# Kernel optimization log

Measured on AMD Instinct MI355X. Metric: run time of the kernel, lower is better.

## Reference

```python
import jax, jax.numpy as jnp
import numpy as np


def setup_inputs() -> dict:
    key = jax.random.key(0)
    k0, k1, k2, k3 = jax.random.split(key, 4)
    B, N, C = 4, 1024, 64
    x = jax.random.normal(k0, (B, N, C), dtype=jnp.float32)
    # torch nn.Linear weights are [out, in]; all projections are bias-free
    W1 = jax.random.normal(k1, (C, C), dtype=jnp.float32) * (1.0 / np.sqrt(C))
    W2 = jax.random.normal(k2, (C, C), dtype=jnp.float32) * (1.0 / np.sqrt(C))
    w3 = jax.random.normal(k3, (C,), dtype=jnp.float32) * (1.0 / np.sqrt(C))
    return {"x": x, "W1": W1, "W2": W2, "w3": w3}


def reference(x, W1, W2, w3):
    # x: [B, N, C]; torch Linear: y = x @ W.T
    x1 = jnp.einsum("bnc,dc->bnd", x, W1)  # [B, N, C]
    x2 = jnp.einsum("bnc,dc->bnd", x, W2)  # [B, N, C]
    # broadcast-add over node pairs, tanh, project C -> 1: [B, N, N]
    combined = jnp.tanh(x1[:, :, None, :] + x2[:, None, :, :])  # [B, N, N, C]
    att = jnp.einsum("bijc,c->bij", combined, w3)
    return jax.nn.softmax(att, axis=-1)
```

## Files before the change

kernel.cpp:

```cpp
#include <hip/hip_runtime.h>
#include <hip/hip_bf16.h>


#define BATCH 4
#define NN    1024
#define CC    64
#define TI    4
#define BLK   512
#define NCH   (NN / BLK)
#define PP    65
#define PROWS 16

__device__ __forceinline__ float fast_exp2(float x) {
#if __has_builtin(__builtin_amdgcn_exp2f)
    return __builtin_amdgcn_exp2f(x);
#else
    return exp2f(x);
#endif
}
__device__ __forceinline__ float fast_rcp(float x) {
#if __has_builtin(__builtin_amdgcn_rcpf)
    return __builtin_amdgcn_rcpf(x);
#else
    return 1.0f / x;
#endif
}

__global__ __launch_bounds__(256) void proj_kernel(
    const float* __restrict__ x, const float* __restrict__ W1,
    const float* __restrict__ W2, float* __restrict__ e1p,
    float* __restrict__ e2p) {
    __shared__ float w1t[CC * PP];
    __shared__ float w2t[CC * PP];
    __shared__ float xs[PROWS * CC];

    const int tid = threadIdx.x;
    const int r0  = blockIdx.x * PROWS;
    {
        const float4* __restrict__ W1v = (const float4*)W1;
        const float4* __restrict__ W2v = (const float4*)W2;
#pragma unroll
        for (int k = 0; k < 4; ++k) {
            const int fi = k * 256 + tid;
            const int r  = fi >> 4;
            const int c4 = (fi & 15) * 4;
            float4 a = W1v[fi], b = W2v[fi];
            w1t[(c4 + 0) * PP + r] = a.x; w1t[(c4 + 1) * PP + r] = a.y;
            w1t[(c4 + 2) * PP + r] = a.z; w1t[(c4 + 3) * PP + r] = a.w;
            w2t[(c4 + 0) * PP + r] = b.x; w2t[(c4 + 1) * PP + r] = b.y;
            w2t[(c4 + 2) * PP + r] = b.z; w2t[(c4 + 3) * PP + r] = b.w;
        }
        const int rr = tid >> 6, c = tid & 63;
#pragma unroll
        for (int k = 0; k < 4; ++k) {
            const int r = k * 4 + rr;
            xs[r * CC + c] = x[(size_t)(r0 + r) * CC + c];
        }
    }
    __syncthreads();

    const int w    = tid >> 6;
    const int lane = tid & 63;
    const int rb   = w * 4;

    float a1[4] = {0.f, 0.f, 0.f, 0.f};
    float a2[4] = {0.f, 0.f, 0.f, 0.f};
#pragma unroll
    for (int c = 0; c < CC; ++c) {
        const float w1v = w1t[c * PP + lane];
        const float w2v = w2t[c * PP + lane];
        const float x0 = xs[(rb + 0) * CC + c];
        const float x1 = xs[(rb + 1) * CC + c];
        const float x2v = xs[(rb + 2) * CC + c];
        const float x3 = xs[(rb + 3) * CC + c];
        a1[0] = fmaf(x0, w1v, a1[0]);  a2[0] = fmaf(x0, w2v, a2[0]);
        a1[1] = fmaf(x1, w1v, a1[1]);  a2[1] = fmaf(x1, w2v, a2[1]);
        a1[2] = fmaf(x2v, w1v, a1[2]); a2[2] = fmaf(x2v, w2v, a2[2]);
        a1[3] = fmaf(x3, w1v, a1[3]);  a2[3] = fmaf(x3, w2v, a2[3]);
    }
    const float K2 = 2.8853900817779268f;
#pragma unroll
    for (int rr = 0; rr < 4; ++rr) {
        const size_t r = (size_t)(r0 + rb + rr);
        e1p[r * CC + lane] = fast_exp2(fminf(a1[rr] * K2, 15.f));
        e2p[r * CC + lane] = fast_exp2(fminf(a2[rr] * K2, 15.f));
    }
}

__device__ __forceinline__ void step2(float e1a, float e1b, float e2,
                                      float wc, float2& acc) {
    float da = fmaf(e1a, e2, 1.f);
    float db = fmaf(e1b, e2, 1.f);
    float r  = fast_rcp(da * db);
    float t  = wc * r;
    acc.x = fmaf(db, t, acc.x);
    acc.y = fmaf(da, t, acc.y);
}

__global__ __launch_bounds__(BLK) void attn_kernel(
    const float* __restrict__ e1p, const float* __restrict__ e2p,
    const float* __restrict__ w3, float* __restrict__ out) {
    __shared__ float e1t[CC * TI];
    __shared__ float att_lds[TI * NN];

    const int tid = threadIdx.x;
    const int bi  = blockIdx.x;
    const int b   = bi >> 8;
    const int i0  = (bi & 255) * TI;

    if (tid < CC * TI) {
        const int ii = tid >> 6, c = tid & 63;
        e1t[c * TI + ii] = e1p[(size_t)((b << 10) + i0 + ii) * CC + c];
    }
    __syncthreads();

    const float4* __restrict__ w3q = (const float4*)w3;
    float sumw3 = 0.f;
#pragma unroll
    for (int q = 0; q < 16; ++q) {
        float4 t = w3q[q];
        sumw3 += (t.x + t.y) + (t.z + t.w);
    }

    const float* __restrict__ e2b = e2p + ((size_t)b << 10) * CC;
    const float4* e1t4 = (const float4*)e1t;

#pragma unroll 1
    for (int ch = 0; ch < NCH; ++ch) {
        const int j = ch * BLK + tid;
        const float4* __restrict__ row = (const float4*)(e2b + (size_t)j * CC);

        float2 accA = {0.f, 0.f};
        float2 accB = {0.f, 0.f};

#pragma unroll 1
        for (int ct = 0; ct < 4; ++ct) {
#pragma unroll
            for (int q = 0; q < 4; ++q) {
                const float4 ev2 = row[ct * 4 + q];
                const float4 wv  = w3q[ct * 4 + q];
                const float ea[4] = {ev2.x, ev2.y, ev2.z, ev2.w};
                const float wa[4] = {wv.x, wv.y, wv.z, wv.w};
#pragma unroll
                for (int m = 0; m < 4; ++m) {
                    const int c = ct * 16 + q * 4 + m;
                    const float4 ev = e1t4[c];
                    step2(ev.x, ev.y, ea[m], wa[m], accA);
                    step2(ev.z, ev.w, ea[m], wa[m], accB);
                }
            }
        }
        att_lds[0 * NN + j] = fmaf(-2.f, accA.x, sumw3);
        att_lds[1 * NN + j] = fmaf(-2.f, accA.y, sumw3);
        att_lds[2 * NN + j] = fmaf(-2.f, accB.x, sumw3);
        att_lds[3 * NN + j] = fmaf(-2.f, accB.y, sumw3);
    }
    __syncthreads();

    {
        const int w    = tid >> 6;
        const int lane = tid & 63;
        if (w < TI) {
            float v[16];
            float m = -3.4e38f;
#pragma unroll
            for (int k = 0; k < 16; ++k) {
                v[k] = att_lds[w * NN + k * 64 + lane];
                m = fmaxf(m, v[k]);
            }
#pragma unroll
            for (int off = 32; off >= 1; off >>= 1)
                m = fmaxf(m, __shfl_xor(m, off));
            const float L2E = 1.4426950408889634f;
            float s = 0.f;
#pragma unroll
            for (int k = 0; k < 16; ++k) {
                v[k] = fast_exp2((v[k] - m) * L2E);
                s += v[k];
            }
#pragma unroll
            for (int off = 32; off >= 1; off >>= 1)
                s += __shfl_xor(s, off);
            const float rs = fast_rcp(s);
            float* __restrict__ orow = out + (((size_t)(b << 10) + (i0 + w)) << 10);
#pragma unroll
            for (int k = 0; k < 16; ++k) orow[k * 64 + lane] = v[k] * rs;
        }
    }
}

extern "C" void kernel_launch(void* const* d_in, const int* in_sizes, int n_in,
                              void* d_out, int out_size, void* d_ws, size_t ws_size,
                              hipStream_t stream) {
    const float* x  = (const float*)d_in[0];
    const float* W1 = (const float*)d_in[1];
    const float* W2 = (const float*)d_in[2];
    const float* w3 = (const float*)d_in[3];
    float* outp = (float*)d_out;

    float* e1p = (float*)d_ws;
    float* e2p = e1p + (size_t)BATCH * NN * CC;

    proj_kernel<<<dim3(BATCH * NN / PROWS), dim3(256), 0, stream>>>(x, W1, W2, e1p, e2p);
    attn_kernel<<<dim3(BATCH * NN / TI), dim3(BLK), 0, stream>>>(e1p, e2p, w3, outp);
}
```

Baseline: 102.7 us.

## Process two j rows per thread and read e1 rows directly via uniform loads

The attention kernel now handles both 512-wide j chunks in a single pass, so each thread accumulates two j rows at once and reuses the loaded e1 and w3 values across them. The shared-memory staging of the four e1 rows and its barrier are dropped. Those rows are read straight from global memory with wave-uniform addresses, which the compiler can turn into scalar loads. This cuts LDS traffic and loop overhead and exposes more independent work per thread, at the cost of more live registers.

```diff
diff --git a/kernel.cpp b/kernel.cpp
--- a/kernel.cpp
+++ b/kernel.cpp
@@ -7,7 +7,6 @@
 #define CC    64
 #define TI    4
 #define BLK   512
-#define NCH   (NN / BLK)
 #define PP    65
 #define PROWS 16
 
@@ -100,7 +99,6 @@
 __global__ __launch_bounds__(BLK) void attn_kernel(
     const float* __restrict__ e1p, const float* __restrict__ e2p,
     const float* __restrict__ w3, float* __restrict__ out) {
-    __shared__ float e1t[CC * TI];
     __shared__ float att_lds[TI * NN];
 
     const int tid = threadIdx.x;
@@ -108,13 +106,16 @@
     const int b   = bi >> 8;
     const int i0  = (bi & 255) * TI;
 
-    if (tid < CC * TI) {
-        const int ii = tid >> 6, c = tid & 63;
-        e1t[c * TI + ii] = e1p[(size_t)((b << 10) + i0 + ii) * CC + c];
-    }
-    __syncthreads();
-
+    const float4* __restrict__ e1r0 =
+        (const float4*)(e1p + ((size_t)(b << 10) + i0 + 0) * CC);
+    const float4* __restrict__ e1r1 =
+        (const float4*)(e1p + ((size_t)(b << 10) + i0 + 1) * CC);
+    const float4* __restrict__ e1r2 =
+        (const float4*)(e1p + ((size_t)(b << 10) + i0 + 2) * CC);
+    const float4* __restrict__ e1r3 =
+        (const float4*)(e1p + ((size_t)(b << 10) + i0 + 3) * CC);
     const float4* __restrict__ w3q = (const float4*)w3;
+
     float sumw3 = 0.f;
 #pragma unroll
     for (int q = 0; q < 16; ++q) {
@@ -123,38 +124,40 @@
     }
 
     const float* __restrict__ e2b = e2p + ((size_t)b << 10) * CC;
-    const float4* e1t4 = (const float4*)e1t;
+    const int j0 = tid, j1 = tid + BLK;
+    const float4* __restrict__ rowA = (const float4*)(e2b + (size_t)j0 * CC);
+    const float4* __restrict__ rowB = (const float4*)(e2b + (size_t)j1 * CC);
+
+    float2 aA = {0.f, 0.f}, bA = {0.f, 0.f};
+    float2 aB = {0.f, 0.f}, bB = {0.f, 0.f};
 
 #pragma unroll 1
-    for (int ch = 0; ch < NCH; ++ch) {
-        const int j = ch * BLK + tid;
-        const float4* __restrict__ row = (const float4*)(e2b + (size_t)j * CC);
-
-        float2 accA = {0.f, 0.f};
-        float2 accB = {0.f, 0.f};
-
-#pragma unroll 1
-        for (int ct = 0; ct < 4; ++ct) {
-#pragma unroll
-            for (int q = 0; q < 4; ++q) {
-                const float4 ev2 = row[ct * 4 + q];
-                const float4 wv  = w3q[ct * 4 + q];
-                const float ea[4] = {ev2.x, ev2.y, ev2.z, ev2.w};
-                const float wa[4] = {wv.x, wv.y, wv.z, wv.w};
-#pragma unroll
-                for (int m = 0; m < 4; ++m) {
-                    const int c = ct * 16 + q * 4 + m;
-                    const float4 ev = e1t4[c];
-                    step2(ev.x, ev.y, ea[m], wa[m], accA);
-                    step2(ev.z, ev.w, ea[m], wa[m], accB);
-                }
-            }
-        }
-        att_lds[0 * NN + j] = fmaf(-2.f, accA.x, sumw3);
-        att_lds[1 * NN + j] = fmaf(-2.f, accA.y, sumw3);
-        att_lds[2 * NN + j] = fmaf(-2.f, accB.x, sumw3);
-        att_lds[3 * NN + j] = fmaf(-2.f, accB.y, sumw3);
-    }
+    for (int ct = 0; ct < 16; ++ct) {
+        const float4 eA = rowA[ct];
+        const float4 eB = rowB[ct];
+        const float4 p0 = e1r0[ct];
+        const float4 p1 = e1r1[ct];
+        const float4 p2 = e1r2[ct];
+        const float4 p3 = e1r3[ct];
+        const float4 wv = w3q[ct];
+        step2(p0.x, p1.x, eA.x, wv.x, aA);  step2(p2.x, p3.x, eA.x, wv.x, bA);
+        step2(p0.x, p1.x, eB.x, wv.x, aB);  step2(p2.x, p3.x, eB.x, wv.x, bB);
+        step2(p0.y, p1.y, eA.y, wv.y, aA);  step2(p2.y, p3.y, eA.y, wv.y, bA);
+        step2(p0.y, p1.y, eB.y, wv.y, aB);  step2(p2.y, p3.y, eB.y, wv.y, bB);
+        step2(p0.z, p1.z, eA.z, wv.z, aA);  step2(p2.z, p3.z, eA.z, wv.z, bA);
+        step2(p0.z, p1.z, eB.z, wv.z, aB);  step2(p2.z, p3.z, eB.z, wv.z, bB);
+        step2(p0.w, p1.w, eA.w, wv.w, aA);  step2(p2.w, p3.w, eA.w, wv.w, bA);
+        step2(p0.w, p1.w, eB.w, wv.w, aB);  step2(p2.w, p3.w, eB.w, wv.w, bB);
+    }
+
+    att_lds[0 * NN + j0] = fmaf(-2.f, aA.x, sumw3);
+    att_lds[1 * NN + j0] = fmaf(-2.f, aA.y, sumw3);
+    att_lds[2 * NN + j0] = fmaf(-2.f, bA.x, sumw3);
+    att_lds[3 * NN + j0] = fmaf(-2.f, bA.y, sumw3);
+    att_lds[0 * NN + j1] = fmaf(-2.f, aB.x, sumw3);
+    att_lds[1 * NN + j1] = fmaf(-2.f, aB.y, sumw3);
+    att_lds[2 * NN + j1] = fmaf(-2.f, bB.x, sumw3);
+    att_lds[3 * NN + j1] = fmaf(-2.f, bB.y, sumw3);
     __syncthreads();
 
     {
```

After: 132.2 us. +28.7%, slower.

## Register-block four j rows per thread with prefetch and 256-thread blocks

Applied to the files above, without the earlier changes.

Shrinks the attention block to 256 threads, each computing four j columns at once, so every LDS read of e1 and w3 is reused across four e2 rows. The loads for the next channel group are issued one iteration ahead as a software prefetch. w3 is now staged in LDS and all four wavefronts take part in the softmax. The aim is fewer LDS reads per unit of math and better latency hiding, at the cost of many more live registers, which may lower occupancy.

```diff
diff --git a/kernel.cpp b/kernel.cpp
--- a/kernel.cpp
+++ b/kernel.cpp
@@ -6,8 +6,8 @@
 #define NN    1024
 #define CC    64
 #define TI    4
-#define BLK   512
-#define NCH   (NN / BLK)
+#define BLK   256
+#define J4    4
 #define PP    65
 #define PROWS 16
 
@@ -97,10 +97,11 @@
     acc.y = fmaf(da, t, acc.y);
 }
 
-__global__ __launch_bounds__(BLK) void attn_kernel(
+__global__ __launch_bounds__(BLK, 4) void attn_kernel(
     const float* __restrict__ e1p, const float* __restrict__ e2p,
     const float* __restrict__ w3, float* __restrict__ out) {
     __shared__ float e1t[CC * TI];
+    __shared__ float w3s[CC];
     __shared__ float att_lds[TI * NN];
 
     const int tid = threadIdx.x;
@@ -108,9 +109,10 @@
     const int b   = bi >> 8;
     const int i0  = (bi & 255) * TI;
 
-    if (tid < CC * TI) {
+    {
         const int ii = tid >> 6, c = tid & 63;
         e1t[c * TI + ii] = e1p[(size_t)((b << 10) + i0 + ii) * CC + c];
+        if (tid < CC) w3s[tid] = w3[tid];
     }
     __syncthreads();
 
@@ -123,69 +125,94 @@
     }
 
     const float* __restrict__ e2b = e2p + ((size_t)b << 10) * CC;
+    const float4* __restrict__ row0 = (const float4*)(e2b + (size_t)(tid          ) * CC);
+    const float4* __restrict__ row1 = (const float4*)(e2b + (size_t)(tid + 1 * BLK) * CC);
+    const float4* __restrict__ row2 = (const float4*)(e2b + (size_t)(tid + 2 * BLK) * CC);
+    const float4* __restrict__ row3 = (const float4*)(e2b + (size_t)(tid + 3 * BLK) * CC);
     const float4* e1t4 = (const float4*)e1t;
+    const float4* w3s4 = (const float4*)w3s;
+
+    float2 a0A = {0.f,0.f}, a0B = {0.f,0.f};
+    float2 a1A = {0.f,0.f}, a1B = {0.f,0.f};
+    float2 a2A = {0.f,0.f}, a2B = {0.f,0.f};
+    float2 a3A = {0.f,0.f}, a3B = {0.f,0.f};
+
+    float4 c0 = row0[0], c1 = row1[0], c2 = row2[0], c3 = row3[0];
 
 #pragma unroll 1
-    for (int ch = 0; ch < NCH; ++ch) {
-        const int j = ch * BLK + tid;
-        const float4* __restrict__ row = (const float4*)(e2b + (size_t)j * CC);
-
-        float2 accA = {0.f, 0.f};
-        float2 accB = {0.f, 0.f};
-
-#pragma unroll 1
-        for (int ct = 0; ct < 4; ++ct) {
-#pragma unroll
-            for (int q = 0; q < 4; ++q) {
-                const float4 ev2 = row[ct * 4 + q];
-                const float4 wv  = w3q[ct * 4 + q];
-                const float ea[4] = {ev2.x, ev2.y, ev2.z, ev2.w};
-                const float wa[4] = {wv.x, wv.y, wv.z, wv.w};
-#pragma unroll
-                for (int m = 0; m < 4; ++m) {
-                    const int c = ct * 16 + q * 4 + m;
-                    const float4 ev = e1t4[c];
-                    step2(ev.x, ev.y, ea[m], wa[m], accA);
-                    step2(ev.z, ev.w, ea[m], wa[m], accB);
-                }
-            }
-        }
-        att_lds[0 * NN + j] = fmaf(-2.f, accA.x, sumw3);
-        att_lds[1 * NN + j] = fmaf(-2.f, accA.y, sumw3);
-        att_lds[2 * NN + j] = fmaf(-2.f, accB.x, sumw3);
-        att_lds[3 * NN + j] = fmaf(-2.f, accB.y, sumw3);
+    for (int ct = 0; ct < 16; ++ct) {
+        const int nx = (ct < 15) ? ct + 1 : 15;
+        float4 n0 = row0[nx], n1 = row1[nx], n2 = row2[nx], n3 = row3[nx];
+
+        const float4 wv = w3s4[ct];
+        const float ca0[4] = {c0.x, c0.y, c0.z, c0.w};
+        const float ca1[4] = {c1.x, c1.y, c1.z, c1.w};
+        const float ca2[4] = {c2.x, c2.y, c2.z, c2.w};
+        const float ca3[4] = {c3.x, c3.y, c3.z, c3.w};
+        const float wa[4]  = {wv.x, wv.y, wv.z, wv.w};
+#pragma unroll
+        for (int m = 0; m < 4; ++m) {
+            const float4 ev = e1t4[ct * 4 + m];
+            step2(ev.x, ev.y, ca0[m], wa[m], a0A);
+            step2(ev.z, ev.w, ca0[m], wa[m], a0B);
+            step2(ev.x, ev.y, ca1[m], wa[m], a1A);
+            step2(ev.z, ev.w, ca1[m], wa[m], a1B);
+            step2(ev.x, ev.y, ca2[m], wa[m], a2A);
+            step2(ev.z, ev.w, ca2[m], wa[m], a2B);
+            step2(ev.x, ev.y, ca3[m], wa[m], a3A);
+            step2(ev.z, ev.w, ca3[m], wa[m], a3B);
+        }
+        c0 = n0; c1 = n1; c2 = n2; c3 = n3;
+    }
+
+    {
+        const int j0 = tid;
+        att_lds[0 * NN + j0 + 0 * BLK] = fmaf(-2.f, a0A.x, sumw3);
+        att_lds[1 * NN + j0 + 0 * BLK] = fmaf(-2.f, a0A.y, sumw3);
+        att_lds[2 * NN + j0 + 0 * BLK] = fmaf(-2.f, a0B.x, sumw3);
+        att_lds[3 * NN + j0 + 0 * BLK] = fmaf(-2.f, a0B.y, sumw3);
+        att_lds[0 * NN + j0 + 1 * BLK] = fmaf(-2.f, a1A.x, sumw3);
+        att_lds[1 * NN + j0 + 1 * BLK] = fmaf(-2.f, a1A.y, sumw3);
+        att_lds[2 * NN + j0 + 1 * BLK] = fmaf(-2.f, a1B.x, sumw3);
+        att_lds[3 * NN + j0 + 1 * BLK] = fmaf(-2.f, a1B.y, sumw3);
+        att_lds[0 * NN + j0 + 2 * BLK] = fmaf(-2.f, a2A.x, sumw3);
+        att_lds[1 * NN + j0 + 2 * BLK] = fmaf(-2.f, a2A.y, sumw3);
+        att_lds[2 * NN + j0 + 2 * BLK] = fmaf(-2.f, a2B.x, sumw3);
+        att_lds[3 * NN + j0 + 2 * BLK] = fmaf(-2.f, a2B.y, sumw3);
+        att_lds[0 * NN + j0 + 3 * BLK] = fmaf(-2.f, a3A.x, sumw3);
+        att_lds[1 * NN + j0 + 3 * BLK] = fmaf(-2.f, a3A.y, sumw3);
+        att_lds[2 * NN + j0 + 3 * BLK] = fmaf(-2.f, a3B.x, sumw3);
+        att_lds[3 * NN + j0 + 3 * BLK] = fmaf(-2.f, a3B.y, sumw3);
     }
     __syncthreads();
 
     {
         const int w    = tid >> 6;
         const int lane = tid & 63;
-        if (w < TI) {
-            float v[16];
-            float m = -3.4e38f;
-#pragma unroll
-            for (int k = 0; k < 16; ++k) {
-                v[k] = att_lds[w * NN + k * 64 + lane];
-                m = fmaxf(m, v[k]);
-            }
-#pragma unroll
-            for (int off = 32; off >= 1; off >>= 1)
-                m = fmaxf(m, __shfl_xor(m, off));
-            const float L2E = 1.4426950408889634f;
-            float s = 0.f;
-#pragma unroll
-            for (int k = 0; k < 16; ++k) {
-                v[k] = fast_exp2((v[k] - m) * L2E);
-                s += v[k];
-            }
-#pragma unroll
-            for (int off = 32; off >= 1; off >>= 1)
-                s += __shfl_xor(s, off);
-            const float rs = fast_rcp(s);
-            float* __restrict__ orow = out + (((size_t)(b << 10) + (i0 + w)) << 10);
-#pragma unroll
-            for (int k = 0; k < 16; ++k) orow[k * 64 + lane] = v[k] * rs;
-        }
+        float v[16];
+        float m = -3.4e38f;
+#pragma unroll
+        for (int k = 0; k < 16; ++k) {
+            v[k] = att_lds[w * NN + k * 64 + lane];
+            m = fmaxf(m, v[k]);
+        }
+#pragma unroll
+        for (int off = 32; off >= 1; off >>= 1)
+            m = fmaxf(m, __shfl_xor(m, off));
+        const float L2E = 1.4426950408889634f;
+        float s = 0.f;
+#pragma unroll
+        for (int k = 0; k < 16; ++k) {
+            v[k] = fast_exp2((v[k] - m) * L2E);
+            s += v[k];
+        }
+#pragma unroll
+        for (int off = 32; off >= 1; off >>= 1)
+            s += __shfl_xor(s, off);
+        const float rs = fast_rcp(s);
+        float* __restrict__ orow = out + (((size_t)(b << 10) + (i0 + w)) << 10);
+#pragma unroll
+        for (int k = 0; k < 16; ++k) orow[k * 64 + lane] = v[k] * rs;
     }
 }
 
```

Measured after the change: 135.7 us. 1.32x slower.
